# Performance work log

Hardware: AMD Instinct MI355X
Metric: run time of the kernel (lower is better)

Reference implementation:

```python
import jax, jax.numpy as jnp
import numpy as np

N_NODES = 50000
N_EDGES = 800000
F_IN = 64
HID = 64
N_GRAPHS = 256
BN_EPS = 1e-5


def setup_inputs() -> dict:
    key = jax.random.key(0)
    ks = jax.random.split(key, 16)
    inp = {
        'x': jax.random.normal(ks[0], (N_NODES, F_IN), dtype=jnp.float32),
        'edge_index': jax.random.randint(ks[1], (2, N_EDGES), 0, N_NODES, dtype=jnp.int64),
        'edge_weight': jax.random.uniform(ks[2], (N_EDGES,), dtype=jnp.float32),
        'batch': jnp.sort(jax.random.randint(ks[3], (N_NODES,), 0, N_GRAPHS, dtype=jnp.int64)),
    }
    def lin(k, fi, fo):
        s = 1.0 / np.sqrt(fi)
        kw, kb = jax.random.split(k)
        return (jax.random.uniform(kw, (fi, fo), jnp.float32, -s, s),
                jax.random.uniform(kb, (fo,), jnp.float32, -s, s))
    inp['W1'], inp['b1'] = lin(ks[4], F_IN, HID)
    inp['W2'], inp['b2'] = lin(ks[5], HID, HID)
    inp['W3'], inp['b3'] = lin(ks[6], HID, HID)
    inp['fcW1'], inp['fcb1'] = lin(ks[7], HID, HID)
    inp['fcW2'], inp['fcb2'] = lin(ks[8], HID, 1)
    for i, k in zip((1, 2, 3), ks[9:12]):
        inp[f'g{i}'] = jnp.ones((HID,), jnp.float32)
        inp[f'be{i}'] = jnp.zeros((HID,), jnp.float32)
    return inp


def gin_conv(x, src, dst, edge_weight, W, b):
    # weighted scatter-add aggregation: agg[dst] += w_e * x[src]
    msg = x[src] * edge_weight[:, None]            # [E, d]
    agg = jax.ops.segment_sum(msg, dst, num_segments=x.shape[0])  # [N, d]
    return (x + agg) @ W + b                       # GIN eps=0, nn = Linear


def batch_norm(x, gamma, beta):
    mu = jnp.mean(x, axis=0)
    var = jnp.var(x, axis=0)
    return (x - mu) * jax.lax.rsqrt(var + BN_EPS) * gamma + beta


def reference(x, edge_index, edge_weight, batch,
              W1, b1, W2, b2, W3, b3, fcW1, fcb1, fcW2, fcb2,
              g1, be1, g2, be2, g3, be3):
    src, dst = edge_index[0], edge_index[1]
    h = batch_norm(jax.nn.relu(gin_conv(x, src, dst, edge_weight, W1, b1)), g1, be1)
    h = batch_norm(jax.nn.relu(gin_conv(h, src, dst, edge_weight, W2, b2)), g2, be2)
    h = batch_norm(gin_conv(h, src, dst, edge_weight, W3, b3), g3, be3)
    pooled = jax.ops.segment_sum(h, batch, num_segments=N_GRAPHS)  # global_add_pool
    h = jax.nn.relu(pooled)
    h = jax.nn.relu(h @ fcW1 + fcb1)
    # dropout is identity in eval / deterministic reference
    return (h @ fcW2 + fcb2).reshape(-1)
```

## Files before the change

### kernel.cpp

```cpp
#include <hip/hip_runtime.h>
#include <hip/hip_bf16.h>


#define NN 50000
#define NE 800000
#define FD 64
#define NG 256
#define CAP 64
#define NBKT 16
#define BN_EPS 1e-5f

#define NPART 8
#define PSIZE 6250
#define ECHUNK 2048
#define NCHUNK ((NE + ECHUNK - 1) / ECHUNK)
#define NBUILD (NCHUNK * NPART)
#define NCVT   ((NN * 16) / 256)

__device__ __forceinline__ float4 dec4(uint2 a) {
    float4 f;
    f.x = __uint_as_float(a.x << 16);
    f.y = __uint_as_float(a.x & 0xFFFF0000u);
    f.z = __uint_as_float(a.y << 16);
    f.w = __uint_as_float(a.y & 0xFFFF0000u);
    return f;
}
__device__ __forceinline__ unsigned rbf(float f) {
    unsigned u = __float_as_uint(f);
    return (u + 0x7FFFu + ((u >> 16) & 1u)) >> 16;
}
__device__ __forceinline__ uint2 enc4(float4 v) {
    uint2 o;
    o.x = rbf(v.x) | (rbf(v.y) << 16);
    o.y = rbf(v.z) | (rbf(v.w) << 16);
    return o;
}

__global__ __launch_bounds__(256) void build_cvt_kernel(
    const int* __restrict__ src, const int* __restrict__ dst,
    const float* __restrict__ ew, int* __restrict__ cursor,
    unsigned* __restrict__ slots,
    const float4* __restrict__ xin, uint2* __restrict__ xout)
{
    int bid = blockIdx.x;
    int tid = threadIdx.x;
    if (bid < NBUILD) {
        int part  = bid & 7;
        int chunk = bid >> 3;
        int base  = chunk * ECHUNK;
        #pragma unroll
        for (int i = 0; i < ECHUNK; i += 256) {
            int e = base + i + tid;
            if (e < NE) {
                int d = dst[e];
                if (d / PSIZE == part) {
                    int pos = atomicAdd(&cursor[d], 1) & (CAP - 1);
                    slots[(size_t)d * CAP + pos] =
                        ((unsigned)src[e] << 16) | rbf(ew[e]);
                }
            }
        }
    } else {
        int i = (bid - NBUILD) * 256 + tid;
        xout[i] = enc4(xin[i]);
    }
}

__global__ __launch_bounds__(64) void bn_affine_kernel(
    const float* __restrict__ bk,
    const float* __restrict__ gamma, const float* __restrict__ beta,
    float* __restrict__ afc)
{
    int t = threadIdx.x;
    float S1 = 0.f, S2 = 0.f;
    #pragma unroll
    for (int i = 0; i < NBKT; i++) {
        S1 += bk[i * 128 + t];
        S2 += bk[i * 128 + FD + t];
    }
    float mu  = S1 * (1.f / NN);
    float var = S2 * (1.f / NN) - mu * mu;
    float a = gamma[t] * rsqrtf(var + BN_EPS);
    afc[t]      = a;
    afc[FD + t] = beta[t] - mu * a;
}

template<int MODE>
__global__ __launch_bounds__(256) void agg_layer_kernel(
    const uint2* __restrict__ h, const int* __restrict__ deg,
    const unsigned* __restrict__ slots,
    const float* __restrict__ afc,
    const float* __restrict__ W, const float* __restrict__ b,
    uint2* __restrict__ y, float* __restrict__ buckets,
    const int* __restrict__ batch, float* __restrict__ pooled)
{
    __shared__ float Ws[FD * FD];
    __shared__ float ps1[4][FD];
    __shared__ float ps2[4][FD];
    int tid  = threadIdx.x;
    int wave = tid >> 6, lane = tid & 63;
    int g = lane >> 4, l = lane & 15;
    int node = blockIdx.x * 4 + wave;

    const float4* __restrict__ Wg = (const float4*)W;
    float4 wr0 = Wg[tid];
    float4 wr1 = Wg[tid + 256];
    float4 wr2 = Wg[tid + 512];
    float4 wr3 = Wg[tid + 768];

    unsigned ms = slots[(size_t)node * CAP + lane];
    int dg = deg[node];
    float4 self = dec4(h[(size_t)node * 16 + l]);
    if (dg > CAP) dg = CAP;

    float4 af, cf;
    if (MODE != 0) {
        af = ((const float4*)afc)[l];
        cf = ((const float4*)afc)[16 + l];
    }

    float4 acc = make_float4(0.f, 0.f, 0.f, 0.f);
    float wsum = 0.f;
    int nIter = (dg + 15) >> 4;
    for (int i = 0; i < nIter; i++) {
        unsigned m[4]; uint2 r[4];
        #pragma unroll
        for (int j = 0; j < 4; j++)
            m[j] = (unsigned)__shfl((int)ms, 16 * i + 4 * j + g, 64);
        #pragma unroll
        for (int j = 0; j < 4; j++)
            r[j] = h[(size_t)(m[j] >> 16) * 16 + l];
        #pragma unroll
        for (int j = 0; j < 4; j++) {
            float w = __uint_as_float(m[j] << 16);
            float4 v = dec4(r[j]);
            wsum += w;
            acc.x = fmaf(w, v.x, acc.x); acc.y = fmaf(w, v.y, acc.y);
            acc.z = fmaf(w, v.z, acc.z); acc.w = fmaf(w, v.w, acc.w);
        }
    }
    acc.x += __shfl_xor(acc.x, 16, 64); acc.y += __shfl_xor(acc.y, 16, 64);
    acc.z += __shfl_xor(acc.z, 16, 64); acc.w += __shfl_xor(acc.w, 16, 64);
    wsum  += __shfl_xor(wsum, 16, 64);
    acc.x += __shfl_xor(acc.x, 32, 64); acc.y += __shfl_xor(acc.y, 32, 64);
    acc.z += __shfl_xor(acc.z, 32, 64); acc.w += __shfl_xor(acc.w, 32, 64);
    wsum  += __shfl_xor(wsum, 32, 64);

    float4 raw;
    raw.x = self.x + acc.x; raw.y = self.y + acc.y;
    raw.z = self.z + acc.z; raw.w = self.w + acc.w;

    float4 hin;
    if (MODE != 0) {
        float sw = 1.0f + wsum;
        hin.x = fmaf(af.x, raw.x, cf.x * sw);
        hin.y = fmaf(af.y, raw.y, cf.y * sw);
        hin.z = fmaf(af.z, raw.z, cf.z * sw);
        hin.w = fmaf(af.w, raw.w, cf.w * sw);
    } else {
        hin = raw;
    }

    {
        float4* Wv = (float4*)Ws;
        Wv[tid]       = wr0;
        Wv[tid + 256] = wr1;
        Wv[tid + 512] = wr2;
        Wv[tid + 768] = wr3;
    }
    __syncthreads();

    const float4* __restrict__ WsV = (const float4*)Ws;
    float4 yp = make_float4(0.f, 0.f, 0.f, 0.f);
    #pragma unroll
    for (int kk = 0; kk < 4; kk++) {
        int srcl = 4 * g + kk;
        float a0 = __shfl(hin.x, srcl, 64);
        float a1 = __shfl(hin.y, srcl, 64);
        float a2 = __shfl(hin.z, srcl, 64);
        float a3 = __shfl(hin.w, srcl, 64);
        int k0 = 16 * g + 4 * kk;
        float4 w0 = WsV[(k0 + 0) * 16 + l];
        float4 w1 = WsV[(k0 + 1) * 16 + l];
        float4 w2 = WsV[(k0 + 2) * 16 + l];
        float4 w3 = WsV[(k0 + 3) * 16 + l];
        yp.x = fmaf(a0, w0.x, yp.x); yp.y = fmaf(a0, w0.y, yp.y);
        yp.z = fmaf(a0, w0.z, yp.z); yp.w = fmaf(a0, w0.w, yp.w);
        yp.x = fmaf(a1, w1.x, yp.x); yp.y = fmaf(a1, w1.y, yp.y);
        yp.z = fmaf(a1, w1.z, yp.z); yp.w = fmaf(a1, w1.w, yp.w);
        yp.x = fmaf(a2, w2.x, yp.x); yp.y = fmaf(a2, w2.y, yp.y);
        yp.z = fmaf(a2, w2.z, yp.z); yp.w = fmaf(a2, w2.w, yp.w);
        yp.x = fmaf(a3, w3.x, yp.x); yp.y = fmaf(a3, w3.y, yp.y);
        yp.z = fmaf(a3, w3.z, yp.z); yp.w = fmaf(a3, w3.w, yp.w);
    }
    yp.x += __shfl_xor(yp.x, 16, 64); yp.y += __shfl_xor(yp.y, 16, 64);
    yp.z += __shfl_xor(yp.z, 16, 64); yp.w += __shfl_xor(yp.w, 16, 64);
    yp.x += __shfl_xor(yp.x, 32, 64); yp.y += __shfl_xor(yp.y, 32, 64);
    yp.z += __shfl_xor(yp.z, 32, 64); yp.w += __shfl_xor(yp.w, 32, 64);

    float4 bias = ((const float4*)b)[l];
    float4 yv;
    yv.x = yp.x + bias.x; yv.y = yp.y + bias.y;
    yv.z = yp.z + bias.z; yv.w = yp.w + bias.w;
    if (MODE < 2) {
        yv.x = fmaxf(yv.x, 0.f); yv.y = fmaxf(yv.y, 0.f);
        yv.z = fmaxf(yv.z, 0.f); yv.w = fmaxf(yv.w, 0.f);
    }
    if (g == 0) {
        if (MODE < 2)
            y[(size_t)node * 16 + l] = enc4(yv);
        ((float4*)&ps1[wave][0])[l] = yv;
        float4 sq;
        sq.x = yv.x * yv.x; sq.y = yv.y * yv.y;
        sq.z = yv.z * yv.z; sq.w = yv.w * yv.w;
        ((float4*)&ps2[wave][0])[l] = sq;
    }
    __syncthreads();
    if (tid < FD) {
        float a = ps1[0][tid] + ps1[1][tid] + ps1[2][tid] + ps1[3][tid];
        float q = ps2[0][tid] + ps2[1][tid] + ps2[2][tid] + ps2[3][tid];
        float* bk = buckets + (blockIdx.x & (NBKT - 1)) * 128;
        atomicAdd(&bk[tid], a);
        atomicAdd(&bk[FD + tid], q);
        if (MODE == 2) {
            int n0 = blockIdx.x * 4;
            int b0 = batch[n0], b3 = batch[n0 + 3];
            if (b0 == b3) {
                atomicAdd(&pooled[b0 * FD + tid], a);
            } else {
                #pragma unroll
                for (int w = 0; w < 4; w++)
                    atomicAdd(&pooled[batch[n0 + w] * FD + tid],
                              ps1[w][tid]);
            }
        }
    }
}

__global__ __launch_bounds__(256) void head_kernel(
    const float* __restrict__ pooled, const int* __restrict__ batch,
    const float* __restrict__ buckets3,
    const float* __restrict__ g3, const float* __restrict__ be3,
    const float* __restrict__ fcW1, const float* __restrict__ fcb1,
    const float* __restrict__ fcW2, const float* __restrict__ fcb2,
    float* __restrict__ out)
{
    __shared__ float red[8][FD];
    __shared__ int bounds[2];
    int tid = threadIdx.x;
    int g = blockIdx.x;

    {
        int f = tid & 63, q = tid >> 6;
        float S1 = 0.f, S2 = 0.f;
        #pragma unroll
        for (int i = 0; i < 4; i++) {
            int bkt = q * 4 + i;
            S1 += buckets3[bkt * 128 + f];
            S2 += buckets3[bkt * 128 + FD + f];
        }
        red[q][f]     = S1;
        red[4 + q][f] = S2;
    }
    if (tid < 2) {
        int target = g + tid;
        int lo = 0, hi = NN;
        while (lo < hi) {
            int mid = (lo + hi) >> 1;
            if (batch[mid] < target) lo = mid + 1; else hi = mid;
        }
        bounds[tid] = lo;
    }
    __syncthreads();

    if (tid < 64) {
        float s1 = red[0][tid] + red[1][tid] + red[2][tid] + red[3][tid];
        float s2 = red[4][tid] + red[5][tid] + red[6][tid] + red[7][tid];
        float mu  = s1 * (1.f / NN);
        float var = s2 * (1.f / NN) - mu * mu;
        float a = g3[tid] * rsqrtf(var + BN_EPS);
        float c = be3[tid] - mu * a;

        float cnt = (float)(bounds[1] - bounds[0]);
        float p = pooled[g * FD + tid];
        p = fmaf(a, p, c * cnt);
        p = fmaxf(p, 0.f);
        float acc1 = fcb1[tid];
        #pragma unroll
        for (int k = 0; k < FD; k++) {
            float pk = __shfl(p, k, 64);
            acc1 = fmaf(pk, fcW1[k * FD + tid], acc1);
        }
        acc1 = fmaxf(acc1, 0.f);
        float prod = acc1 * fcW2[tid];
        #pragma unroll
        for (int off = 32; off > 0; off >>= 1)
            prod += __shfl_xor(prod, off, 64);
        if (tid == 0) out[g] = prod + fcb2[0];
    }
}

extern "C" void kernel_launch(void* const* d_in, const int* in_sizes, int n_in,
                              void* d_out, int out_size, void* d_ws, size_t ws_size,
                              hipStream_t stream) {
    const float* x     = (const float*)d_in[0];
    const int*   ei    = (const int*)d_in[1];
    const float* ew    = (const float*)d_in[2];
    const int*   batch = (const int*)d_in[3];
    const float* W1 = (const float*)d_in[4],  *b1 = (const float*)d_in[5];
    const float* W2 = (const float*)d_in[6],  *b2 = (const float*)d_in[7];
    const float* W3 = (const float*)d_in[8],  *b3 = (const float*)d_in[9];
    const float* fcW1 = (const float*)d_in[10], *fcb1 = (const float*)d_in[11];
    const float* fcW2 = (const float*)d_in[12], *fcb2 = (const float*)d_in[13];
    const float* g1 = (const float*)d_in[14], *be1 = (const float*)d_in[15];
    const float* g2 = (const float*)d_in[16], *be2 = (const float*)d_in[17];
    const float* g3 = (const float*)d_in[18], *be3 = (const float*)d_in[19];
    float* out = (float*)d_out;

    const int* srcp = ei;
    const int* dstp = ei + NE;

    char* ws = (char*)d_ws;
    size_t off = 0;
    auto take = [&](size_t bytes) -> char* {
        char* p = ws + off;
        off += (bytes + 255) & ~(size_t)255;
        return p;
    };
    uint2*    xbf   = (uint2*)   take((size_t)NN * FD * 2);
    uint2*    bufA  = (uint2*)   take((size_t)NN * FD * 2);
    uint2*    bufB  = (uint2*)   take((size_t)NN * FD * 2);
    float*    afc1  = (float*)   take((size_t)128 * 4);
    float*    afc2  = (float*)   take((size_t)128 * 4);
    size_t zero_base = off;
    unsigned* slots = (unsigned*)take((size_t)NN * CAP * 4);
    int*      cursor= (int*)     take((size_t)NN * 4);
    float*    buckets=(float*)   take((size_t)3 * NBKT * 128 * 4);
    float*    pooled =(float*)   take((size_t)NG * FD * 4);
    size_t zero_bytes = off - zero_base;
    (void)ws_size; (void)n_in; (void)in_sizes; (void)out_size;

    hipMemsetAsync(ws + zero_base, 0, zero_bytes, stream);

    build_cvt_kernel<<<NBUILD + NCVT, 256, 0, stream>>>(srcp, dstp, ew,
                                                        cursor, slots,
                                                        (const float4*)x, xbf);

    const int gridA = NN / 4;

    float* bk1 = buckets + 0 * NBKT * 128;
    float* bk2 = buckets + 1 * NBKT * 128;
    float* bk3 = buckets + 2 * NBKT * 128;

    agg_layer_kernel<0><<<gridA, 256, 0, stream>>>(xbf, cursor, slots,
                                                   nullptr,
                                                   W1, b1, bufA, bk1,
                                                   nullptr, nullptr);
    bn_affine_kernel<<<1, 64, 0, stream>>>(bk1, g1, be1, afc1);
    agg_layer_kernel<1><<<gridA, 256, 0, stream>>>(bufA, cursor, slots,
                                                   afc1,
                                                   W2, b2, bufB, bk2,
                                                   nullptr, nullptr);
    bn_affine_kernel<<<1, 64, 0, stream>>>(bk2, g2, be2, afc2);
    agg_layer_kernel<2><<<gridA, 256, 0, stream>>>(bufB, cursor, slots,
                                                   afc2,
                                                   W3, b3, nullptr, bk3,
                                                   batch, pooled);
    head_kernel<<<NG, 256, 0, stream>>>(pooled, batch, bk3, g3, be3,
                                        fcW1, fcb1, fcW2, fcb2, out);
}
```

Before: 263.7 us.

## Fold BN-affine computation into aggregation kernels and use 512-thread blocks

Removes the two single-block bn_affine launches. Each wave of the next aggregation layer now recomputes the batch-norm scale and shift from the previous layer's bucket sums and broadcasts them with shuffles. Blocks also grow from 4 to 8 nodes (512 threads), which halves how many times each block loads the weight matrix into shared memory and halves the bucket and pool atomics. The cost is redundant per-wave reads of the 16 buckets plus rsqrt work, and larger blocks that may lower occupancy flexibility.

Measured after the change: 271.9 us. 3.1% more time.

```diff
diff --git a/kernel.cpp b/kernel.cpp
--- a/kernel.cpp
+++ b/kernel.cpp
@@ -66,47 +66,27 @@
     }
 }
 
-__global__ __launch_bounds__(64) void bn_affine_kernel(
-    const float* __restrict__ bk,
-    const float* __restrict__ gamma, const float* __restrict__ beta,
-    float* __restrict__ afc)
-{
-    int t = threadIdx.x;
-    float S1 = 0.f, S2 = 0.f;
-    #pragma unroll
-    for (int i = 0; i < NBKT; i++) {
-        S1 += bk[i * 128 + t];
-        S2 += bk[i * 128 + FD + t];
-    }
-    float mu  = S1 * (1.f / NN);
-    float var = S2 * (1.f / NN) - mu * mu;
-    float a = gamma[t] * rsqrtf(var + BN_EPS);
-    afc[t]      = a;
-    afc[FD + t] = beta[t] - mu * a;
-}
-
 template<int MODE>
-__global__ __launch_bounds__(256) void agg_layer_kernel(
+__global__ __launch_bounds__(512) void agg_layer_kernel(
     const uint2* __restrict__ h, const int* __restrict__ deg,
     const unsigned* __restrict__ slots,
-    const float* __restrict__ afc,
+    const float* __restrict__ prev_bk,
+    const float* __restrict__ prev_gamma, const float* __restrict__ prev_beta,
     const float* __restrict__ W, const float* __restrict__ b,
     uint2* __restrict__ y, float* __restrict__ buckets,
     const int* __restrict__ batch, float* __restrict__ pooled)
 {
     __shared__ float Ws[FD * FD];
-    __shared__ float ps1[4][FD];
-    __shared__ float ps2[4][FD];
+    __shared__ float ps1[8][FD];
+    __shared__ float ps2[8][FD];
     int tid  = threadIdx.x;
     int wave = tid >> 6, lane = tid & 63;
     int g = lane >> 4, l = lane & 15;
-    int node = blockIdx.x * 4 + wave;
+    int node = blockIdx.x * 8 + wave;
 
     const float4* __restrict__ Wg = (const float4*)W;
     float4 wr0 = Wg[tid];
-    float4 wr1 = Wg[tid + 256];
-    float4 wr2 = Wg[tid + 512];
-    float4 wr3 = Wg[tid + 768];
+    float4 wr1 = Wg[tid + 512];
 
     unsigned ms = slots[(size_t)node * CAP + lane];
     int dg = deg[node];
@@ -115,8 +95,20 @@
 
     float4 af, cf;
     if (MODE != 0) {
-        af = ((const float4*)afc)[l];
-        cf = ((const float4*)afc)[16 + l];
+        float S1 = 0.f, S2 = 0.f;
+        #pragma unroll
+        for (int i = 0; i < NBKT; i++) {
+            S1 += prev_bk[i * 128 + lane];
+            S2 += prev_bk[i * 128 + FD + lane];
+        }
+        float mu  = S1 * (1.f / NN);
+        float var = S2 * (1.f / NN) - mu * mu;
+        float a = prev_gamma[lane] * rsqrtf(var + BN_EPS);
+        float c = prev_beta[lane] - mu * a;
+        af.x = __shfl(a, 4 * l + 0, 64); af.y = __shfl(a, 4 * l + 1, 64);
+        af.z = __shfl(a, 4 * l + 2, 64); af.w = __shfl(a, 4 * l + 3, 64);
+        cf.x = __shfl(c, 4 * l + 0, 64); cf.y = __shfl(c, 4 * l + 1, 64);
+        cf.z = __shfl(c, 4 * l + 2, 64); cf.w = __shfl(c, 4 * l + 3, 64);
     }
 
     float4 acc = make_float4(0.f, 0.f, 0.f, 0.f);
@@ -164,9 +156,7 @@
     {
         float4* Wv = (float4*)Ws;
         Wv[tid]       = wr0;
-        Wv[tid + 256] = wr1;
-        Wv[tid + 512] = wr2;
-        Wv[tid + 768] = wr3;
+        Wv[tid + 512] = wr1;
     }
     __syncthreads();
 
@@ -217,21 +207,25 @@
     }
     __syncthreads();
     if (tid < FD) {
-        float a = ps1[0][tid] + ps1[1][tid] + ps1[2][tid] + ps1[3][tid];
-        float q = ps2[0][tid] + ps2[1][tid] + ps2[2][tid] + ps2[3][tid];
+        float a = 0.f, q = 0.f;
+        #pragma unroll
+        for (int wv = 0; wv < 8; wv++) {
+            a += ps1[wv][tid];
+            q += ps2[wv][tid];
+        }
         float* bk = buckets + (blockIdx.x & (NBKT - 1)) * 128;
         atomicAdd(&bk[tid], a);
         atomicAdd(&bk[FD + tid], q);
         if (MODE == 2) {
-            int n0 = blockIdx.x * 4;
-            int b0 = batch[n0], b3 = batch[n0 + 3];
-            if (b0 == b3) {
+            int n0 = blockIdx.x * 8;
+            int b0 = batch[n0], b7 = batch[n0 + 7];
+            if (b0 == b7) {
                 atomicAdd(&pooled[b0 * FD + tid], a);
             } else {
                 #pragma unroll
-                for (int w = 0; w < 4; w++)
-                    atomicAdd(&pooled[batch[n0 + w] * FD + tid],
-                              ps1[w][tid]);
+                for (int wv = 0; wv < 8; wv++)
+                    atomicAdd(&pooled[batch[n0 + wv] * FD + tid],
+                              ps1[wv][tid]);
             }
         }
     }
@@ -330,8 +324,6 @@
     uint2*    xbf   = (uint2*)   take((size_t)NN * FD * 2);
     uint2*    bufA  = (uint2*)   take((size_t)NN * FD * 2);
     uint2*    bufB  = (uint2*)   take((size_t)NN * FD * 2);
-    float*    afc1  = (float*)   take((size_t)128 * 4);
-    float*    afc2  = (float*)   take((size_t)128 * 4);
     size_t zero_base = off;
     unsigned* slots = (unsigned*)take((size_t)NN * CAP * 4);
     int*      cursor= (int*)     take((size_t)NN * 4);
@@ -346,24 +338,22 @@
                                                         cursor, slots,
                                                         (const float4*)x, xbf);
 
-    const int gridA = NN / 4;
+    const int gridA = NN / 8;
 
     float* bk1 = buckets + 0 * NBKT * 128;
     float* bk2 = buckets + 1 * NBKT * 128;
     float* bk3 = buckets + 2 * NBKT * 128;
 
-    agg_layer_kernel<0><<<gridA, 256, 0, stream>>>(xbf, cursor, slots,
-                                                   nullptr,
+    agg_layer_kernel<0><<<gridA, 512, 0, stream>>>(xbf, cursor, slots,
+                                                   nullptr, nullptr, nullptr,
                                                    W1, b1, bufA, bk1,
                                                    nullptr, nullptr);
-    bn_affine_kernel<<<1, 64, 0, stream>>>(bk1, g1, be1, afc1);
-    agg_layer_kernel<1><<<gridA, 256, 0, stream>>>(bufA, cursor, slots,
-                                                   afc1,
+    agg_layer_kernel<1><<<gridA, 512, 0, stream>>>(bufA, cursor, slots,
+                                                   bk1, g1, be1,
                                                    W2, b2, bufB, bk2,
                                                    nullptr, nullptr);
-    bn_affine_kernel<<<1, 64, 0, stream>>>(bk2, g2, be2, afc2);
-    agg_layer_kernel<2><<<gridA, 256, 0, stream>>>(bufB, cursor, slots,
-                                                   afc2,
+    agg_layer_kernel<2><<<gridA, 512, 0, stream>>>(bufB, cursor, slots,
+                                                   bk2, g2, be2,
                                                    W3, b3, nullptr, bk3,
                                                    batch, pooled);
     head_kernel<<<NG, 256, 0, stream>>>(pooled, batch, bk3, g3, be3,
```
